# Performance work log

Hardware: AMD Instinct MI355X
Metric: run time of the kernel (lower is better)

Reference implementation:

```python
import jax, jax.numpy as jnp
import numpy as np

N_CELLS, IN_DIM, HID, OUT = 65536, 128, 256, 128
MLP_H = 128   # engine MLP hidden width is hard-coded to 128 in the source
N_MORPH = 32  # min(32, n_cells//4)


def setup_inputs() -> dict:
    key = jax.random.key(0)
    ks = jax.random.split(key, 18)
    s = 0.05
    return {
        "x": jax.random.normal(ks[0], (1, IN_DIM), jnp.float32),
        "hiddens": jax.random.normal(ks[1], (N_CELLS, HID), jnp.float32) * 0.1,
        "Wa1": jax.random.normal(ks[2], (MLP_H, IN_DIM + HID), jnp.float32) * s,
        "ba1": jax.random.normal(ks[3], (MLP_H,), jnp.float32) * s,
        "Wa2": jax.random.normal(ks[4], (OUT, MLP_H), jnp.float32) * s,
        "ba2": jax.random.normal(ks[5], (OUT,), jnp.float32) * s,
        "Wg1": jax.random.normal(ks[6], (MLP_H, IN_DIM + HID), jnp.float32) * s,
        "bg1": jax.random.normal(ks[7], (MLP_H,), jnp.float32) * s,
        "Wg2": jax.random.normal(ks[8], (OUT, MLP_H), jnp.float32) * s,
        "bg2": jax.random.normal(ks[9], (OUT,), jnp.float32) * s,
        "W_ih": jax.random.normal(ks[10], (3 * HID, OUT + 1), jnp.float32) * s,
        "W_hh": jax.random.normal(ks[11], (3 * HID, HID), jnp.float32) * s,
        "b_ih": jax.random.normal(ks[12], (3 * HID,), jnp.float32) * s,
        "b_hh": jax.random.normal(ks[13], (3 * HID,), jnp.float32) * s,
        "nat_w": jnp.eye(HID, dtype=jnp.float32),  # nn.init.eye_
        "morph_w": jax.random.normal(ks[14], (N_MORPH, HID, HID), jnp.float32) * 0.02,
        "morph_src": jax.random.randint(ks[15], (N_MORPH,), 0, N_CELLS, jnp.int32),
        "morph_tgt": jax.random.randint(ks[16], (N_MORPH,), 0, N_CELLS, jnp.int32),
        "step": 0,
    }


def _forward(x, hiddens, Wa1, ba1, Wa2, ba2, Wg1, bg1, Wg2, bg2,
             W_ih, W_hh, b_ih, b_hh, nat_w, morph_w, morph_src, morph_tgt, step):
    n = hiddens.shape[0]
    # --- BenchMind, batched over all cells (x broadcast to every cell) ---
    xb = jnp.broadcast_to(x, (n, x.shape[-1]))
    combined = jnp.concatenate([xb, hiddens], axis=-1)               # [n, in+hid]
    a = jax.nn.relu(combined @ Wa1.T + ba1) @ Wa2.T + ba2            # [n, out]
    g = jax.nn.relu(combined @ Wg1.T + bg1) @ Wg2.T + bg2            # [n, out]
    out = a - g                                                       # [n, out]
    tension = jnp.mean(out * out, axis=-1, keepdims=True)            # [n, 1]
    # mem_input is detached in torch
    mem_in = jax.lax.stop_gradient(jnp.concatenate([out, tension], axis=-1))
    # --- PyTorch GRUCell math ---
    gi = mem_in @ W_ih.T + b_ih                                      # [n, 3H]
    gh = hiddens @ W_hh.T + b_hh                                     # [n, 3H]
    i_r, i_z, i_n = jnp.split(gi, 3, axis=-1)
    h_r, h_z, h_n = jnp.split(gh, 3, axis=-1)
    r = jax.nn.sigmoid(i_r + h_r)
    z = jax.nn.sigmoid(i_z + h_z)
    nn_ = jnp.tanh(i_n + r * h_n)
    hid = jax.lax.stop_gradient((1.0 - z) * nn_ + z * hiddens)       # detached new hiddens
    if step % 3 == 0:
        hid = jax.lax.stop_gradient(hid @ nat_w.T)                   # natural transformation
    # --- limit / colimit (morphism gather-transform-aggregate) ---
    limit = jnp.einsum('mij,mj->i', morph_w, hid[morph_src]) / N_MORPH
    colimit = jnp.einsum('mji,mj->i', morph_w, hid[morph_tgt]) / N_MORPH
    diff = limit - colimit
    cat_tension = jnp.mean(diff * diff)
    hid = hid + 0.05 * jax.lax.stop_gradient(diff)[None, :]
    # --- faction sync (+ debate if step > 5) ---
    n_f = min(8, n // 2)
    fs = n // n_f
    hf = hid[: n_f * fs].reshape(n_f, fs, hid.shape[-1])
    fmean = hf.mean(axis=1, keepdims=True)                           # [n_f,1,H]
    hf = 0.85 * hf + 0.15 * fmean
    if step > 5:
        global_op = hf.mean(axis=1).mean(axis=0)                     # mean of faction means
        dc = max(1, fs // 4)
        hf = hf.at[:, :dc].set(0.85 * hf[:, :dc] + 0.15 * global_op)
    hid = jnp.concatenate([hf.reshape(n_f * fs, -1), hid[n_f * fs:]], axis=0)
    # --- tension-weighted combination (weights detached: .item() in torch) ---
    t = jax.lax.stop_gradient(tension[:, 0])                         # [n]
    w = jax.nn.softmax(t, axis=0)
    combined_out = jnp.sum(w[:, None] * out, axis=0, keepdims=True)  # [1, out]
    avg_tension = jnp.mean(tension) + 0.1 * cat_tension
    return combined_out, avg_tension, hid


def reference(x, hiddens, Wa1, ba1, Wa2, ba2, Wg1, bg1, Wg2, bg2,
              W_ih, W_hh, b_ih, b_hh, nat_w, morph_w, morph_src, morph_tgt, step):
    combined_out, avg_tension, _ = _forward(
        x, hiddens, Wa1, ba1, Wa2, ba2, Wg1, bg1, Wg2, bg2,
        W_ih, W_hh, b_ih, b_hh, nat_w, morph_w, morph_src, morph_tgt, step)
    return combined_out, avg_tension
```

## Files before the change

### kernel.cpp

```cpp
#include <hip/hip_runtime.h>
#include <math.h>

#define OFF_W1B   0
#define OFF_W2A   32768
#define OFF_XW1B  49152
#define OFF_B2D   49408
#define OFF_PT    49536
#define OFF_PE    51584
#define OFF_POUT  53632
#define OFF_MI4   315776
#define OFF_TEN   323968
#define OFF_HH4   324032
#define OFF_GI    340416
#define OFF_GH    389568
#define OFF_PLIM  438720
#define OFF_PCOL8 446912
#define OFF_GMSK  512448

typedef short bf16x8 __attribute__((ext_vector_type(8)));
typedef short s16x4  __attribute__((ext_vector_type(4)));
typedef float f32x4  __attribute__((ext_vector_type(4)));

__device__ __forceinline__ unsigned short f2bf(float f) {
    unsigned u = __builtin_bit_cast(unsigned, f);
    u += 0x7FFFu + ((u >> 16) & 1u);
    return (unsigned short)(u >> 16);
}

__device__ __forceinline__ bf16x8 cvt8(float4 a, float4 b) {
    bf16x8 v;
    v[0] = (short)f2bf(a.x); v[1] = (short)f2bf(a.y);
    v[2] = (short)f2bf(a.z); v[3] = (short)f2bf(a.w);
    v[4] = (short)f2bf(b.x); v[5] = (short)f2bf(b.y);
    v[6] = (short)f2bf(b.z); v[7] = (short)f2bf(b.w);
    return v;
}

__global__ __launch_bounds__(256) void k_prep(
    const float* __restrict__ x, const float* __restrict__ hiddens,
    const float* __restrict__ Wa1, const float* __restrict__ ba1,
    const float* __restrict__ Wa2, const float* __restrict__ ba2,
    const float* __restrict__ Wg1, const float* __restrict__ bg1,
    const float* __restrict__ Wg2, const float* __restrict__ bg2,
    const int* __restrict__ msrc, const int* __restrict__ mtgt,
    float* __restrict__ ws)
{
    const int b = blockIdx.x, t = threadIdx.x;
    unsigned short* w1b = (unsigned short*)(ws + OFF_W1B);
    unsigned short* w2a = (unsigned short*)(ws + OFF_W2A);
    if (b < 256) {
        const int n = b;
        const float* row = (n < 128) ? &Wa1[n * 384] : &Wg1[(n - 128) * 384];
        const int kc = t >> 3;
        w1b[(kc * 256 + n) * 8 + (t & 7)] = f2bf(row[128 + t]);
        if (n < 128) {
            float w2 = (t < 128) ? Wa2[n * 128 + t] : -Wg2[n * 128 + (t - 128)];
            w2a[(kc * 128 + n) * 8 + (t & 7)] = f2bf(w2);
        }
    } else if (b == 256) {
        const int n = t;
        const float* wr = (n < 128) ? &Wa1[n * 384] : &Wg1[(n - 128) * 384];
        float s = (n < 128) ? ba1[n] : bg1[n - 128];
        for (int j = 0; j < 128; ++j) s = fmaf(x[j], wr[j], s);
        ws[OFF_XW1B + n] = s;
        if (n < 128) ws[OFF_B2D + n] = ba2[n] - bg2[n];
    } else if (b == 257) {
        unsigned* gm = (unsigned*)(ws + OFF_GMSK);
        for (int i = t; i < 2048; i += 256) gm[i] = 0u;
        __syncthreads();
        if (t < 64) {
            const int cell = (t < 32) ? msrc[t] : mtgt[t - 32];
            atomicOr(&gm[cell >> 5], 1u << (cell & 31));
        }
    } else {
        const int g = b - 258;
        const int cell = (g < 32) ? msrc[g] : mtgt[g - 32];
        ws[OFF_HH4 + (t >> 2) * 256 + g * 4 + (t & 3)] = hiddens[(size_t)cell * 256 + t];
    }
}

__global__ __launch_bounds__(256, 2) void k_main(
    const float* __restrict__ hiddens,
    const int* __restrict__ msrc, const int* __restrict__ mtgt,
    float* __restrict__ ws)
{
    __shared__ __align__(16) short hB[32 * 256];
    __shared__ __align__(16) short h1B[32 * 256];
    __shared__ float part[128];
    __shared__ float e_sm[32], t_sm_[32];
    __shared__ int gid_sm[64];

    const int tid  = threadIdx.x;
    const int lane = tid & 63, wid = tid >> 6;
    const int l15 = lane & 15, l4 = lane >> 4;
    const int bt = blockIdx.x;

    if (tid < 64) gid_sm[tid] = (tid < 32) ? msrc[tid] : mtgt[tid - 32];

    const uint4* w1g = (const uint4*)(ws + OFF_W1B);
    const uint4* w2g = (const uint4*)(ws + OFF_W2A);
    const unsigned* gm = (const unsigned*)(ws + OFF_GMSK);

    {
        const int rc = tid >> 3;
        const float* hsrc = hiddens + (size_t)(bt * 32 + rc) * 256 + (tid & 7) * 32;
        float4 v0 = *(const float4*)(hsrc + 0);
        float4 v1 = *(const float4*)(hsrc + 4);
        float4 v2 = *(const float4*)(hsrc + 8);
        float4 v3 = *(const float4*)(hsrc + 12);
        float4 v4 = *(const float4*)(hsrc + 16);
        float4 v5 = *(const float4*)(hsrc + 20);
        float4 v6 = *(const float4*)(hsrc + 24);
        float4 v7 = *(const float4*)(hsrc + 28);
        const int kc0 = (tid & 7) * 4;
        *(bf16x8*)&hB[rc * 256 + (((kc0 + 0) ^ (rc & 15)) << 3)] = cvt8(v0, v1);
        *(bf16x8*)&hB[rc * 256 + (((kc0 + 1) ^ (rc & 15)) << 3)] = cvt8(v2, v3);
        *(bf16x8*)&hB[rc * 256 + (((kc0 + 2) ^ (rc & 15)) << 3)] = cvt8(v4, v5);
        *(bf16x8*)&hB[rc * 256 + (((kc0 + 3) ^ (rc & 15)) << 3)] = cvt8(v6, v7);
    }
    __syncthreads();

    const int wb1 = wid * 64 + l15;
    uint4 c0 = w1g[(0 + l4) * 256 + wb1 + 0];
    uint4 c1 = w1g[(0 + l4) * 256 + wb1 + 16];
    uint4 c2 = w1g[(0 + l4) * 256 + wb1 + 32];
    uint4 c3 = w1g[(0 + l4) * 256 + wb1 + 48];
    uint4 p0 = w1g[(4 + l4) * 256 + wb1 + 0];
    uint4 p1 = w1g[(4 + l4) * 256 + wb1 + 16];
    uint4 p2 = w1g[(4 + l4) * 256 + wb1 + 32];
    uint4 p3 = w1g[(4 + l4) * 256 + wb1 + 48];
    uint4 g2c0, g2c1, g2p0, g2p1;

    f32x4 acc[4][2];
#pragma unroll
    for (int q = 0; q < 4; ++q)
#pragma unroll
        for (int ct = 0; ct < 2; ++ct) acc[q][ct] = (f32x4)0.f;

    __builtin_amdgcn_s_setprio(1);
#pragma unroll
    for (int s = 0; s < 8; ++s) {
        uint4 f0, f1, f2, f3;
        if (s < 6) {
            f0 = w1g[((s + 2) * 4 + l4) * 256 + wb1 + 0];
            f1 = w1g[((s + 2) * 4 + l4) * 256 + wb1 + 16];
            f2 = w1g[((s + 2) * 4 + l4) * 256 + wb1 + 32];
            f3 = w1g[((s + 2) * 4 + l4) * 256 + wb1 + 48];
        } else if (s == 6) {
            g2c0 = w2g[(0 + l4) * 128 + wid * 32 + l15];
            g2c1 = w2g[(0 + l4) * 128 + wid * 32 + 16 + l15];
        } else {
            g2p0 = w2g[(4 + l4) * 128 + wid * 32 + l15];
            g2p1 = w2g[(4 + l4) * 128 + wid * 32 + 16 + l15];
        }
        bf16x8 bfr0 = *(const bf16x8*)&hB[(0 * 16 + l15) * 256 + (((s * 4 + l4) ^ l15) << 3)];
        bf16x8 bfr1 = *(const bf16x8*)&hB[(1 * 16 + l15) * 256 + (((s * 4 + l4) ^ l15) << 3)];
        acc[0][0] = __builtin_amdgcn_mfma_f32_16x16x32_bf16(__builtin_bit_cast(bf16x8, c0), bfr0, acc[0][0], 0, 0, 0);
        acc[0][1] = __builtin_amdgcn_mfma_f32_16x16x32_bf16(__builtin_bit_cast(bf16x8, c0), bfr1, acc[0][1], 0, 0, 0);
        acc[1][0] = __builtin_amdgcn_mfma_f32_16x16x32_bf16(__builtin_bit_cast(bf16x8, c1), bfr0, acc[1][0], 0, 0, 0);
        acc[1][1] = __builtin_amdgcn_mfma_f32_16x16x32_bf16(__builtin_bit_cast(bf16x8, c1), bfr1, acc[1][1], 0, 0, 0);
        acc[2][0] = __builtin_amdgcn_mfma_f32_16x16x32_bf16(__builtin_bit_cast(bf16x8, c2), bfr0, acc[2][0], 0, 0, 0);
        acc[2][1] = __builtin_amdgcn_mfma_f32_16x16x32_bf16(__builtin_bit_cast(bf16x8, c2), bfr1, acc[2][1], 0, 0, 0);
        acc[3][0] = __builtin_amdgcn_mfma_f32_16x16x32_bf16(__builtin_bit_cast(bf16x8, c3), bfr0, acc[3][0], 0, 0, 0);
        acc[3][1] = __builtin_amdgcn_mfma_f32_16x16x32_bf16(__builtin_bit_cast(bf16x8, c3), bfr1, acc[3][1], 0, 0, 0);
        c0 = p0; c1 = p1; c2 = p2; c3 = p3;
        if (s < 6) { p0 = f0; p1 = f1; p2 = f2; p3 = f3; }
    }
    __builtin_amdgcn_s_setprio(0);

#pragma unroll
    for (int nt = 0; nt < 4; ++nt) {
        const int n0 = wid * 64 + nt * 16 + l4 * 4;
        float4 xb = *(const float4*)(ws + OFF_XW1B + n0);
        const float bx[4] = {xb.x, xb.y, xb.z, xb.w};
        const int chunk = n0 >> 3;
        const int off = (l4 & 1) * 4;
#pragma unroll
        for (int ct = 0; ct < 2; ++ct) {
            const int c = ct * 16 + l15;
            s16x4 pk;
#pragma unroll
            for (int r = 0; r < 4; ++r)
                pk[r] = (short)f2bf(fmaxf(acc[nt][ct][r] + bx[r], 0.f));
            *(s16x4*)&h1B[c * 256 + ((chunk ^ l15) << 3) + off] = pk;
        }
    }
    __syncthreads();

    f32x4 acc2[2][2];
#pragma unroll
    for (int ot = 0; ot < 2; ++ot)
#pragma unroll
        for (int ct = 0; ct < 2; ++ct) acc2[ot][ct] = (f32x4)0.f;

    __builtin_amdgcn_s_setprio(1);
#pragma unroll
    for (int s = 0; s < 8; ++s) {
        uint4 f0, f1;
        if (s < 6) {
            f0 = w2g[((s + 2) * 4 + l4) * 128 + wid * 32 + l15];
            f1 = w2g[((s + 2) * 4 + l4) * 128 + wid * 32 + 16 + l15];
        }
        bf16x8 b20 = *(const bf16x8*)&h1B[(0 * 16 + l15) * 256 + (((s * 4 + l4) ^ l15) << 3)];
        bf16x8 b21 = *(const bf16x8*)&h1B[(1 * 16 + l15) * 256 + (((s * 4 + l4) ^ l15) << 3)];
        acc2[0][0] = __builtin_amdgcn_mfma_f32_16x16x32_bf16(__builtin_bit_cast(bf16x8, g2c0), b20, acc2[0][0], 0, 0, 0);
        acc2[0][1] = __builtin_amdgcn_mfma_f32_16x16x32_bf16(__builtin_bit_cast(bf16x8, g2c0), b21, acc2[0][1], 0, 0, 0);
        acc2[1][0] = __builtin_amdgcn_mfma_f32_16x16x32_bf16(__builtin_bit_cast(bf16x8, g2c1), b20, acc2[1][0], 0, 0, 0);
        acc2[1][1] = __builtin_amdgcn_mfma_f32_16x16x32_bf16(__builtin_bit_cast(bf16x8, g2c1), b21, acc2[1][1], 0, 0, 0);
        g2c0 = g2p0; g2c1 = g2p1;
        if (s < 6) { g2p0 = f0; g2p1 = f1; }
    }
    __builtin_amdgcn_s_setprio(0);

    float outv[2][2][4];
#pragma unroll
    for (int ot = 0; ot < 2; ++ot) {
        float4 bd = *(const float4*)(ws + OFF_B2D + wid * 32 + ot * 16 + l4 * 4);
        const float bv[4] = {bd.x, bd.y, bd.z, bd.w};
#pragma unroll
        for (int ct = 0; ct < 2; ++ct)
#pragma unroll
            for (int r = 0; r < 4; ++r)
                outv[ot][ct][r] = acc2[ot][ct][r] + bv[r];
    }

#pragma unroll
    for (int ct = 0; ct < 2; ++ct) {
        float sq = 0.f;
#pragma unroll
        for (int ot = 0; ot < 2; ++ot)
#pragma unroll
            for (int r = 0; r < 4; ++r)
                sq = fmaf(outv[ot][ct][r], outv[ot][ct][r], sq);
        sq += __shfl_xor(sq, 16);
        sq += __shfl_xor(sq, 32);
        if (l4 == 0) part[wid * 32 + ct * 16 + l15] = sq;
    }
    __syncthreads();

    if (tid < 32) {
        float s = part[tid] + part[32 + tid] + part[64 + tid] + part[96 + tid];
        const float tv = s * (1.f / 128.f);
        const float ev = expf(tv);
        t_sm_[tid] = tv; e_sm[tid] = ev;
        float pt = tv, pe = ev;
        for (int off = 16; off > 0; off >>= 1) {
            pt += __shfl_down(pt, off);
            pe += __shfl_down(pe, off);
        }
        if (tid == 0) { ws[OFF_PT + bt] = pt; ws[OFF_PE + bt] = pe; }
        unsigned m = gm[bt];
        while (m) {
            const int g = __builtin_ctz(m); m &= m - 1;
            const int cg = gid_sm[g];
            if ((cg >> 5) == bt && (cg & 31) == tid) ws[OFF_TEN + g] = tv;
        }
    }
    __syncthreads();

    {
        float p[2][4];
#pragma unroll
        for (int ot = 0; ot < 2; ++ot)
#pragma unroll
            for (int r = 0; r < 4; ++r) {
                float s = e_sm[l15] * outv[ot][0][r];
                s = fmaf(e_sm[16 + l15], outv[ot][1][r], s);
                p[ot][r] = s;
            }
#pragma unroll
        for (int ot = 0; ot < 2; ++ot)
#pragma unroll
            for (int r = 0; r < 4; ++r) {
                p[ot][r] += __shfl_xor(p[ot][r], 1);
                p[ot][r] += __shfl_xor(p[ot][r], 2);
                p[ot][r] += __shfl_xor(p[ot][r], 4);
                p[ot][r] += __shfl_xor(p[ot][r], 8);
            }
        if (l15 == 0) {
#pragma unroll
            for (int ot = 0; ot < 2; ++ot)
                *(float4*)(ws + OFF_POUT + (size_t)bt * 128 + wid * 32 + ot * 16 + l4 * 4) =
                    make_float4(p[ot][0], p[ot][1], p[ot][2], p[ot][3]);
        }
    }
    {
        unsigned m = gm[bt];
        while (m) {
            const int g = __builtin_ctz(m); m &= m - 1;
            const int cg = gid_sm[g];
            if ((cg >> 5) != bt) continue;
            const int c = cg & 31;
            if ((c & 15) == l15) {
                const int ct = c >> 4;
#pragma unroll
                for (int ot = 0; ot < 2; ++ot)
                    *(float4*)(ws + OFF_MI4 + (wid * 8 + ot * 4 + l4) * 256 + g * 4) =
                        make_float4(outv[ot][ct][0], outv[ot][ct][1],
                                    outv[ot][ct][2], outv[ot][ct][3]);
            }
        }
    }
}

__global__ __launch_bounds__(256) void k_tail1(
    const float* __restrict__ W_ih, const float* __restrict__ W_hh,
    const float* __restrict__ b_ih, const float* __restrict__ b_hh,
    float* __restrict__ ws)
{
    const int lane = threadIdx.x & 63;
    const int w    = threadIdx.x >> 6;
    const int row  = __builtin_amdgcn_readfirstlane(blockIdx.x * 4 + w);
    const float* mi4 = ws + OFF_MI4;
    const float* hh4 = ws + OFF_HH4;

    const float* wi = W_ih + row * 129;
    float gi = b_ih[row];
#pragma unroll 8
    for (int q = 0; q < 32; ++q) {
        float4 a = *(const float4*)(mi4 + q * 256 + lane * 4);
        gi = fmaf(wi[4 * q + 0], a.x, gi);
        gi = fmaf(wi[4 * q + 1], a.y, gi);
        gi = fmaf(wi[4 * q + 2], a.z, gi);
        gi = fmaf(wi[4 * q + 3], a.w, gi);
    }
    gi = fmaf(ws[OFF_TEN + lane], wi[128], gi);

    const float* wh = W_hh + (size_t)row * 256;
    float gh = b_hh[row];
#pragma unroll 8
    for (int q = 0; q < 64; ++q) {
        float4 a = *(const float4*)(hh4 + q * 256 + lane * 4);
        float4 b = *(const float4*)(wh + 4 * q);
        gh = fmaf(b.x, a.x, gh);
        gh = fmaf(b.y, a.y, gh);
        gh = fmaf(b.z, a.z, gh);
        gh = fmaf(b.w, a.w, gh);
    }
    ws[OFF_GI + lane * 768 + row] = gi;
    ws[OFF_GH + lane * 768 + row] = gh;
}

__global__ __launch_bounds__(256) void k_morph(
    const float* __restrict__ morph_w, const float* __restrict__ nat_w,
    const int* __restrict__ step, float* __restrict__ ws)
{
    __shared__ float wsm[32 * 264];
    __shared__ float hd0[256], hd1[256];
    __shared__ float hs[256], ht[256];
    const int blk = blockIdx.x, t = threadIdx.x;
    const int m = blk >> 3, ch = blk & 7;
    const float* wm = morph_w + (size_t)m * 65536 + (size_t)ch * 32 * 256;
    {
        const int r = t >> 3, c0 = (t & 7) * 32;
#pragma unroll
        for (int it = 0; it < 8; ++it)
            *(float4*)&wsm[r * 264 + c0 + it * 4] = *(const float4*)(wm + r * 256 + c0 + it * 4);
    }
#pragma unroll
    for (int h = 0; h < 2; ++h) {
        const int g = h * 32 + m;
        const float i_r = ws[OFF_GI + g * 768 + t];
        const float i_z = ws[OFF_GI + g * 768 + 256 + t];
        const float i_n = ws[OFF_GI + g * 768 + 512 + t];
        const float h_r = ws[OFF_GH + g * 768 + t];
        const float h_z = ws[OFF_GH + g * 768 + 256 + t];
        const float h_n = ws[OFF_GH + g * 768 + 512 + t];
        const float hv  = ws[OFF_HH4 + (t >> 2) * 256 + g * 4 + (t & 3)];
        const float r  = 1.f / (1.f + expf(-(i_r + h_r)));
        const float z  = 1.f / (1.f + expf(-(i_z + h_z)));
        const float nn = tanhf(i_n + r * h_n);
        const float hid = (1.f - z) * nn + z * hv;
        if (h == 0) hd0[t] = hid; else hd1[t] = hid;
    }
    __syncthreads();

    float hn0, hn1;
    if (step[0] % 3 == 0) {
        const float4* wr = (const float4*)(nat_w + (size_t)t * 256);
        float s0 = 0.f, s1 = 0.f;
        for (int q = 0; q < 64; ++q) {
            float4 wq = wr[q];
            s0 = fmaf(wq.x, hd0[4 * q + 0], s0); s1 = fmaf(wq.x, hd1[4 * q + 0], s1);
            s0 = fmaf(wq.y, hd0[4 * q + 1], s0); s1 = fmaf(wq.y, hd1[4 * q + 1], s1);
            s0 = fmaf(wq.z, hd0[4 * q + 2], s0); s1 = fmaf(wq.z, hd1[4 * q + 2], s1);
            s0 = fmaf(wq.w, hd0[4 * q + 3], s0); s1 = fmaf(wq.w, hd1[4 * q + 3], s1);
        }
        hn0 = s0; hn1 = s1;
    } else {
        hn0 = hd0[t]; hn1 = hd1[t];
    }
    hs[t] = hn0; ht[t] = hn1;
    __syncthreads();

    {
        const int il = t >> 3, jc = t & 7;
        float L = 0.f;
#pragma unroll 8
        for (int jj = 0; jj < 32; ++jj) {
            const int j = jc + 8 * jj;
            L = fmaf(wsm[il * 264 + j], hs[j], L);
        }
        L += __shfl_down(L, 4);
        L += __shfl_down(L, 2);
        L += __shfl_down(L, 1);
        if (jc == 0) ws[OFF_PLIM + m * 256 + ch * 32 + il] = L;
    }
    {
        float C = 0.f;
#pragma unroll 8
        for (int r = 0; r < 32; ++r)
            C = fmaf(wsm[r * 264 + t], ht[ch * 32 + r], C);
        ws[OFF_PCOL8 + blk * 256 + t] = C;
    }
}

__global__ __launch_bounds__(256) void k_out(const float* __restrict__ ws,
                                             float* __restrict__ out)
{
    __shared__ float red[256];
    const int b = blockIdx.x, t = threadIdx.x;
    if (b < 128) {
        float so = 0.f, se = 0.f;
        for (int i = t; i < 2048; i += 256) {
            so += ws[OFF_POUT + (size_t)i * 128 + b];
            se += ws[OFF_PE + i];
        }
        red[t] = so; __syncthreads();
        for (int s = 128; s > 0; s >>= 1) { if (t < s) red[t] += red[t + s]; __syncthreads(); }
        const float SO = red[0]; __syncthreads();
        red[t] = se; __syncthreads();
        for (int s = 128; s > 0; s >>= 1) { if (t < s) red[t] += red[t + s]; __syncthreads(); }
        if (t == 0) out[b] = SO / red[0];
    } else {
        float pt = 0.f;
        for (int i = t; i < 2048; i += 256) pt += ws[OFF_PT + i];
        float L = 0.f, C = 0.f;
        for (int m = 0; m < 32; ++m) L += ws[OFF_PLIM + m * 256 + t];
        for (int mc = 0; mc < 256; ++mc) C += ws[OFF_PCOL8 + mc * 256 + t];
        const float d = (L - C) * (1.f / 32.f);
        red[t] = d * d; __syncthreads();
        for (int s = 128; s > 0; s >>= 1) { if (t < s) red[t] += red[t + s]; __syncthreads(); }
        const float cat = red[0] * (1.f / 256.f); __syncthreads();
        red[t] = pt; __syncthreads();
        for (int s = 128; s > 0; s >>= 1) { if (t < s) red[t] += red[t + s]; __syncthreads(); }
        if (t == 0) out[128] = red[0] * (1.f / 65536.f) + 0.1f * cat;
    }
}

extern "C" void kernel_launch(void* const* d_in, const int* in_sizes, int n_in,
                              void* d_out, int out_size, void* d_ws, size_t ws_size,
                              hipStream_t stream)
{
    const float* x     = (const float*)d_in[0];
    const float* hidd  = (const float*)d_in[1];
    const float* Wa1   = (const float*)d_in[2];
    const float* ba1   = (const float*)d_in[3];
    const float* Wa2   = (const float*)d_in[4];
    const float* ba2   = (const float*)d_in[5];
    const float* Wg1   = (const float*)d_in[6];
    const float* bg1   = (const float*)d_in[7];
    const float* Wg2   = (const float*)d_in[8];
    const float* bg2   = (const float*)d_in[9];
    const float* W_ih  = (const float*)d_in[10];
    const float* W_hh  = (const float*)d_in[11];
    const float* b_ih  = (const float*)d_in[12];
    const float* b_hh  = (const float*)d_in[13];
    const float* nat_w = (const float*)d_in[14];
    const float* mw    = (const float*)d_in[15];
    const int*   msrc  = (const int*)d_in[16];
    const int*   mtgt  = (const int*)d_in[17];
    const int*   step  = (const int*)d_in[18];

    float* out = (float*)d_out;
    float* ws  = (float*)d_ws;

    k_prep <<<322, 256, 0, stream>>>(x, hidd, Wa1, ba1, Wa2, ba2, Wg1, bg1, Wg2, bg2, msrc, mtgt, ws);
    k_main <<<2048, 256, 0, stream>>>(hidd, msrc, mtgt, ws);
    k_tail1<<<192, 256, 0, stream>>>(W_ih, W_hh, b_ih, b_hh, ws);
    k_morph<<<256, 256, 0, stream>>>(mw, nat_w, step, ws);
    k_out  <<<129, 256, 0, stream>>>(ws, out);
}
```

Before: 76.17 us.

## Process two 32-cell tiles per k_main block with prefetched second tile

Each k_main block now handles 64 cells as two sequential 32-row tiles, halving the grid to 1024 blocks. The second tile's hidden rows are loaded into registers at the start and converted into a second LDS buffer while the first tile's layer-1 epilogue runs, so their load latency overlaps compute. Launch bounds are raised to 3 blocks per SM. The cost is more LDS per block, higher register pressure from the prefetched values, and fewer blocks for latency hiding.

Measured after the change: 82.87 us. +8.8%, slower.

```diff
diff --git a/kernel.cpp b/kernel.cpp
--- a/kernel.cpp
+++ b/kernel.cpp
@@ -79,12 +79,12 @@
     }
 }
 
-__global__ __launch_bounds__(256, 2) void k_main(
+__global__ __launch_bounds__(256, 3) void k_main(
     const float* __restrict__ hiddens,
     const int* __restrict__ msrc, const int* __restrict__ mtgt,
     float* __restrict__ ws)
 {
-    __shared__ __align__(16) short hB[32 * 256];
+    __shared__ __align__(16) short hB[2][32 * 256];
     __shared__ __align__(16) short h1B[32 * 256];
     __shared__ float part[128];
     __shared__ float e_sm[32], t_sm_[32];
@@ -93,7 +93,7 @@
     const int tid  = threadIdx.x;
     const int lane = tid & 63, wid = tid >> 6;
     const int l15 = lane & 15, l4 = lane >> 4;
-    const int bt = blockIdx.x;
+    const int blk = blockIdx.x;
 
     if (tid < 64) gid_sm[tid] = (tid < 32) ? msrc[tid] : mtgt[tid - 32];
 
@@ -101,9 +101,11 @@
     const uint4* w2g = (const uint4*)(ws + OFF_W2A);
     const unsigned* gm = (const unsigned*)(ws + OFF_GMSK);
 
+    const int rc = tid >> 3;
+    const int kc0 = (tid & 7) * 4;
+    const float* hsrc = hiddens + (size_t)(blk * 64 + rc) * 256 + (tid & 7) * 32;
+
     {
-        const int rc = tid >> 3;
-        const float* hsrc = hiddens + (size_t)(bt * 32 + rc) * 256 + (tid & 7) * 32;
         float4 v0 = *(const float4*)(hsrc + 0);
         float4 v1 = *(const float4*)(hsrc + 4);
         float4 v2 = *(const float4*)(hsrc + 8);
@@ -112,194 +114,215 @@
         float4 v5 = *(const float4*)(hsrc + 20);
         float4 v6 = *(const float4*)(hsrc + 24);
         float4 v7 = *(const float4*)(hsrc + 28);
-        const int kc0 = (tid & 7) * 4;
-        *(bf16x8*)&hB[rc * 256 + (((kc0 + 0) ^ (rc & 15)) << 3)] = cvt8(v0, v1);
-        *(bf16x8*)&hB[rc * 256 + (((kc0 + 1) ^ (rc & 15)) << 3)] = cvt8(v2, v3);
-        *(bf16x8*)&hB[rc * 256 + (((kc0 + 2) ^ (rc & 15)) << 3)] = cvt8(v4, v5);
-        *(bf16x8*)&hB[rc * 256 + (((kc0 + 3) ^ (rc & 15)) << 3)] = cvt8(v6, v7);
-    }
+        *(bf16x8*)&hB[0][rc * 256 + (((kc0 + 0) ^ (rc & 15)) << 3)] = cvt8(v0, v1);
+        *(bf16x8*)&hB[0][rc * 256 + (((kc0 + 1) ^ (rc & 15)) << 3)] = cvt8(v2, v3);
+        *(bf16x8*)&hB[0][rc * 256 + (((kc0 + 2) ^ (rc & 15)) << 3)] = cvt8(v4, v5);
+        *(bf16x8*)&hB[0][rc * 256 + (((kc0 + 3) ^ (rc & 15)) << 3)] = cvt8(v6, v7);
+    }
+    float4 n0 = *(const float4*)(hsrc + 8192 + 0);
+    float4 n1 = *(const float4*)(hsrc + 8192 + 4);
+    float4 n2 = *(const float4*)(hsrc + 8192 + 8);
+    float4 n3 = *(const float4*)(hsrc + 8192 + 12);
+    float4 n4 = *(const float4*)(hsrc + 8192 + 16);
+    float4 n5 = *(const float4*)(hsrc + 8192 + 20);
+    float4 n6 = *(const float4*)(hsrc + 8192 + 24);
+    float4 n7 = *(const float4*)(hsrc + 8192 + 28);
     __syncthreads();
 
     const int wb1 = wid * 64 + l15;
-    uint4 c0 = w1g[(0 + l4) * 256 + wb1 + 0];
-    uint4 c1 = w1g[(0 + l4) * 256 + wb1 + 16];
-    uint4 c2 = w1g[(0 + l4) * 256 + wb1 + 32];
-    uint4 c3 = w1g[(0 + l4) * 256 + wb1 + 48];
-    uint4 p0 = w1g[(4 + l4) * 256 + wb1 + 0];
-    uint4 p1 = w1g[(4 + l4) * 256 + wb1 + 16];
-    uint4 p2 = w1g[(4 + l4) * 256 + wb1 + 32];
-    uint4 p3 = w1g[(4 + l4) * 256 + wb1 + 48];
-    uint4 g2c0, g2c1, g2p0, g2p1;
-
-    f32x4 acc[4][2];
-#pragma unroll
-    for (int q = 0; q < 4; ++q)
-#pragma unroll
-        for (int ct = 0; ct < 2; ++ct) acc[q][ct] = (f32x4)0.f;
-
-    __builtin_amdgcn_s_setprio(1);
-#pragma unroll
-    for (int s = 0; s < 8; ++s) {
-        uint4 f0, f1, f2, f3;
-        if (s < 6) {
-            f0 = w1g[((s + 2) * 4 + l4) * 256 + wb1 + 0];
-            f1 = w1g[((s + 2) * 4 + l4) * 256 + wb1 + 16];
-            f2 = w1g[((s + 2) * 4 + l4) * 256 + wb1 + 32];
-            f3 = w1g[((s + 2) * 4 + l4) * 256 + wb1 + 48];
-        } else if (s == 6) {
-            g2c0 = w2g[(0 + l4) * 128 + wid * 32 + l15];
-            g2c1 = w2g[(0 + l4) * 128 + wid * 32 + 16 + l15];
-        } else {
-            g2p0 = w2g[(4 + l4) * 128 + wid * 32 + l15];
-            g2p1 = w2g[(4 + l4) * 128 + wid * 32 + 16 + l15];
-        }
-        bf16x8 bfr0 = *(const bf16x8*)&hB[(0 * 16 + l15) * 256 + (((s * 4 + l4) ^ l15) << 3)];
-        bf16x8 bfr1 = *(const bf16x8*)&hB[(1 * 16 + l15) * 256 + (((s * 4 + l4) ^ l15) << 3)];
-        acc[0][0] = __builtin_amdgcn_mfma_f32_16x16x32_bf16(__builtin_bit_cast(bf16x8, c0), bfr0, acc[0][0], 0, 0, 0);
-        acc[0][1] = __builtin_amdgcn_mfma_f32_16x16x32_bf16(__builtin_bit_cast(bf16x8, c0), bfr1, acc[0][1], 0, 0, 0);
-        acc[1][0] = __builtin_amdgcn_mfma_f32_16x16x32_bf16(__builtin_bit_cast(bf16x8, c1), bfr0, acc[1][0], 0, 0, 0);
-        acc[1][1] = __builtin_amdgcn_mfma_f32_16x16x32_bf16(__builtin_bit_cast(bf16x8, c1), bfr1, acc[1][1], 0, 0, 0);
-        acc[2][0] = __builtin_amdgcn_mfma_f32_16x16x32_bf16(__builtin_bit_cast(bf16x8, c2), bfr0, acc[2][0], 0, 0, 0);
-        acc[2][1] = __builtin_amdgcn_mfma_f32_16x16x32_bf16(__builtin_bit_cast(bf16x8, c2), bfr1, acc[2][1], 0, 0, 0);
-        acc[3][0] = __builtin_amdgcn_mfma_f32_16x16x32_bf16(__builtin_bit_cast(bf16x8, c3), bfr0, acc[3][0], 0, 0, 0);
-        acc[3][1] = __builtin_amdgcn_mfma_f32_16x16x32_bf16(__builtin_bit_cast(bf16x8, c3), bfr1, acc[3][1], 0, 0, 0);
-        c0 = p0; c1 = p1; c2 = p2; c3 = p3;
-        if (s < 6) { p0 = f0; p1 = f1; p2 = f2; p3 = f3; }
-    }
-    __builtin_amdgcn_s_setprio(0);
-
-#pragma unroll
-    for (int nt = 0; nt < 4; ++nt) {
-        const int n0 = wid * 64 + nt * 16 + l4 * 4;
-        float4 xb = *(const float4*)(ws + OFF_XW1B + n0);
-        const float bx[4] = {xb.x, xb.y, xb.z, xb.w};
-        const int chunk = n0 >> 3;
-        const int off = (l4 & 1) * 4;
+
+#pragma unroll
+    for (int t = 0; t < 2; ++t) {
+        const int bt = blk * 2 + t;
+        const short* hBt = hB[t];
+
+        uint4 c0 = w1g[(0 + l4) * 256 + wb1 + 0];
+        uint4 c1 = w1g[(0 + l4) * 256 + wb1 + 16];
+        uint4 c2 = w1g[(0 + l4) * 256 + wb1 + 32];
+        uint4 c3 = w1g[(0 + l4) * 256 + wb1 + 48];
+        uint4 p0 = w1g[(4 + l4) * 256 + wb1 + 0];
+        uint4 p1 = w1g[(4 + l4) * 256 + wb1 + 16];
+        uint4 p2 = w1g[(4 + l4) * 256 + wb1 + 32];
+        uint4 p3 = w1g[(4 + l4) * 256 + wb1 + 48];
+        uint4 g2c0, g2c1, g2p0, g2p1;
+
+        f32x4 acc[4][2];
+#pragma unroll
+        for (int q = 0; q < 4; ++q)
+#pragma unroll
+            for (int ct = 0; ct < 2; ++ct) acc[q][ct] = (f32x4)0.f;
+
+        __builtin_amdgcn_s_setprio(1);
+#pragma unroll
+        for (int s = 0; s < 8; ++s) {
+            uint4 f0, f1, f2, f3;
+            if (s < 6) {
+                f0 = w1g[((s + 2) * 4 + l4) * 256 + wb1 + 0];
+                f1 = w1g[((s + 2) * 4 + l4) * 256 + wb1 + 16];
+                f2 = w1g[((s + 2) * 4 + l4) * 256 + wb1 + 32];
+                f3 = w1g[((s + 2) * 4 + l4) * 256 + wb1 + 48];
+            } else if (s == 6) {
+                g2c0 = w2g[(0 + l4) * 128 + wid * 32 + l15];
+                g2c1 = w2g[(0 + l4) * 128 + wid * 32 + 16 + l15];
+            } else {
+                g2p0 = w2g[(4 + l4) * 128 + wid * 32 + l15];
+                g2p1 = w2g[(4 + l4) * 128 + wid * 32 + 16 + l15];
+            }
+            bf16x8 bfr0 = *(const bf16x8*)&hBt[(0 * 16 + l15) * 256 + (((s * 4 + l4) ^ l15) << 3)];
+            bf16x8 bfr1 = *(const bf16x8*)&hBt[(1 * 16 + l15) * 256 + (((s * 4 + l4) ^ l15) << 3)];
+            acc[0][0] = __builtin_amdgcn_mfma_f32_16x16x32_bf16(__builtin_bit_cast(bf16x8, c0), bfr0, acc[0][0], 0, 0, 0);
+            acc[0][1] = __builtin_amdgcn_mfma_f32_16x16x32_bf16(__builtin_bit_cast(bf16x8, c0), bfr1, acc[0][1], 0, 0, 0);
+            acc[1][0] = __builtin_amdgcn_mfma_f32_16x16x32_bf16(__builtin_bit_cast(bf16x8, c1), bfr0, acc[1][0], 0, 0, 0);
+            acc[1][1] = __builtin_amdgcn_mfma_f32_16x16x32_bf16(__builtin_bit_cast(bf16x8, c1), bfr1, acc[1][1], 0, 0, 0);
+            acc[2][0] = __builtin_amdgcn_mfma_f32_16x16x32_bf16(__builtin_bit_cast(bf16x8, c2), bfr0, acc[2][0], 0, 0, 0);
+            acc[2][1] = __builtin_amdgcn_mfma_f32_16x16x32_bf16(__builtin_bit_cast(bf16x8, c2), bfr1, acc[2][1], 0, 0, 0);
+            acc[3][0] = __builtin_amdgcn_mfma_f32_16x16x32_bf16(__builtin_bit_cast(bf16x8, c3), bfr0, acc[3][0], 0, 0, 0);
+            acc[3][1] = __builtin_amdgcn_mfma_f32_16x16x32_bf16(__builtin_bit_cast(bf16x8, c3), bfr1, acc[3][1], 0, 0, 0);
+            c0 = p0; c1 = p1; c2 = p2; c3 = p3;
+            if (s < 6) { p0 = f0; p1 = f1; p2 = f2; p3 = f3; }
+        }
+        __builtin_amdgcn_s_setprio(0);
+
+#pragma unroll
+        for (int nt = 0; nt < 4; ++nt) {
+            const int n0i = wid * 64 + nt * 16 + l4 * 4;
+            float4 xb = *(const float4*)(ws + OFF_XW1B + n0i);
+            const float bx[4] = {xb.x, xb.y, xb.z, xb.w};
+            const int chunk = n0i >> 3;
+            const int off = (l4 & 1) * 4;
+#pragma unroll
+            for (int ct = 0; ct < 2; ++ct) {
+                const int c = ct * 16 + l15;
+                s16x4 pk;
+#pragma unroll
+                for (int r = 0; r < 4; ++r)
+                    pk[r] = (short)f2bf(fmaxf(acc[nt][ct][r] + bx[r], 0.f));
+                *(s16x4*)&h1B[c * 256 + ((chunk ^ l15) << 3) + off] = pk;
+            }
+        }
+        if (t == 0) {
+            *(bf16x8*)&hB[1][rc * 256 + (((kc0 + 0) ^ (rc & 15)) << 3)] = cvt8(n0, n1);
+            *(bf16x8*)&hB[1][rc * 256 + (((kc0 + 1) ^ (rc & 15)) << 3)] = cvt8(n2, n3);
+            *(bf16x8*)&hB[1][rc * 256 + (((kc0 + 2) ^ (rc & 15)) << 3)] = cvt8(n4, n5);
+            *(bf16x8*)&hB[1][rc * 256 + (((kc0 + 3) ^ (rc & 15)) << 3)] = cvt8(n6, n7);
+        }
+        __syncthreads();
+
+        f32x4 acc2[2][2];
+#pragma unroll
+        for (int ot = 0; ot < 2; ++ot)
+#pragma unroll
+            for (int ct = 0; ct < 2; ++ct) acc2[ot][ct] = (f32x4)0.f;
+
+        __builtin_amdgcn_s_setprio(1);
+#pragma unroll
+        for (int s = 0; s < 8; ++s) {
+            uint4 f0, f1;
+            if (s < 6) {
+                f0 = w2g[((s + 2) * 4 + l4) * 128 + wid * 32 + l15];
+                f1 = w2g[((s + 2) * 4 + l4) * 128 + wid * 32 + 16 + l15];
+            }
+            bf16x8 b20 = *(const bf16x8*)&h1B[(0 * 16 + l15) * 256 + (((s * 4 + l4) ^ l15) << 3)];
+            bf16x8 b21 = *(const bf16x8*)&h1B[(1 * 16 + l15) * 256 + (((s * 4 + l4) ^ l15) << 3)];
+            acc2[0][0] = __builtin_amdgcn_mfma_f32_16x16x32_bf16(__builtin_bit_cast(bf16x8, g2c0), b20, acc2[0][0], 0, 0, 0);
+            acc2[0][1] = __builtin_amdgcn_mfma_f32_16x16x32_bf16(__builtin_bit_cast(bf16x8, g2c0), b21, acc2[0][1], 0, 0, 0);
+            acc2[1][0] = __builtin_amdgcn_mfma_f32_16x16x32_bf16(__builtin_bit_cast(bf16x8, g2c1), b20, acc2[1][0], 0, 0, 0);
+            acc2[1][1] = __builtin_amdgcn_mfma_f32_16x16x32_bf16(__builtin_bit_cast(bf16x8, g2c1), b21, acc2[1][1], 0, 0, 0);
+            g2c0 = g2p0; g2c1 = g2p1;
+            if (s < 6) { g2p0 = f0; g2p1 = f1; }
+        }
+        __builtin_amdgcn_s_setprio(0);
+
+        float outv[2][2][4];
+#pragma unroll
+        for (int ot = 0; ot < 2; ++ot) {
+            float4 bd = *(const float4*)(ws + OFF_B2D + wid * 32 + ot * 16 + l4 * 4);
+            const float bv[4] = {bd.x, bd.y, bd.z, bd.w};
+#pragma unroll
+            for (int ct = 0; ct < 2; ++ct)
+#pragma unroll
+                for (int r = 0; r < 4; ++r)
+                    outv[ot][ct][r] = acc2[ot][ct][r] + bv[r];
+        }
+
 #pragma unroll
         for (int ct = 0; ct < 2; ++ct) {
-            const int c = ct * 16 + l15;
-            s16x4 pk;
-#pragma unroll
-            for (int r = 0; r < 4; ++r)
-                pk[r] = (short)f2bf(fmaxf(acc[nt][ct][r] + bx[r], 0.f));
-            *(s16x4*)&h1B[c * 256 + ((chunk ^ l15) << 3) + off] = pk;
-        }
-    }
-    __syncthreads();
-
-    f32x4 acc2[2][2];
-#pragma unroll
-    for (int ot = 0; ot < 2; ++ot)
-#pragma unroll
-        for (int ct = 0; ct < 2; ++ct) acc2[ot][ct] = (f32x4)0.f;
-
-    __builtin_amdgcn_s_setprio(1);
-#pragma unroll
-    for (int s = 0; s < 8; ++s) {
-        uint4 f0, f1;
-        if (s < 6) {
-            f0 = w2g[((s + 2) * 4 + l4) * 128 + wid * 32 + l15];
-            f1 = w2g[((s + 2) * 4 + l4) * 128 + wid * 32 + 16 + l15];
-        }
-        bf16x8 b20 = *(const bf16x8*)&h1B[(0 * 16 + l15) * 256 + (((s * 4 + l4) ^ l15) << 3)];
-        bf16x8 b21 = *(const bf16x8*)&h1B[(1 * 16 + l15) * 256 + (((s * 4 + l4) ^ l15) << 3)];
-        acc2[0][0] = __builtin_amdgcn_mfma_f32_16x16x32_bf16(__builtin_bit_cast(bf16x8, g2c0), b20, acc2[0][0], 0, 0, 0);
-        acc2[0][1] = __builtin_amdgcn_mfma_f32_16x16x32_bf16(__builtin_bit_cast(bf16x8, g2c0), b21, acc2[0][1], 0, 0, 0);
-        acc2[1][0] = __builtin_amdgcn_mfma_f32_16x16x32_bf16(__builtin_bit_cast(bf16x8, g2c1), b20, acc2[1][0], 0, 0, 0);
-        acc2[1][1] = __builtin_amdgcn_mfma_f32_16x16x32_bf16(__builtin_bit_cast(bf16x8, g2c1), b21, acc2[1][1], 0, 0, 0);
-        g2c0 = g2p0; g2c1 = g2p1;
-        if (s < 6) { g2p0 = f0; g2p1 = f1; }
-    }
-    __builtin_amdgcn_s_setprio(0);
-
-    float outv[2][2][4];
-#pragma unroll
-    for (int ot = 0; ot < 2; ++ot) {
-        float4 bd = *(const float4*)(ws + OFF_B2D + wid * 32 + ot * 16 + l4 * 4);
-        const float bv[4] = {bd.x, bd.y, bd.z, bd.w};
-#pragma unroll
-        for (int ct = 0; ct < 2; ++ct)
-#pragma unroll
-            for (int r = 0; r < 4; ++r)
-                outv[ot][ct][r] = acc2[ot][ct][r] + bv[r];
-    }
-
-#pragma unroll
-    for (int ct = 0; ct < 2; ++ct) {
-        float sq = 0.f;
-#pragma unroll
-        for (int ot = 0; ot < 2; ++ot)
-#pragma unroll
-            for (int r = 0; r < 4; ++r)
-                sq = fmaf(outv[ot][ct][r], outv[ot][ct][r], sq);
-        sq += __shfl_xor(sq, 16);
-        sq += __shfl_xor(sq, 32);
-        if (l4 == 0) part[wid * 32 + ct * 16 + l15] = sq;
-    }
-    __syncthreads();
-
-    if (tid < 32) {
-        float s = part[tid] + part[32 + tid] + part[64 + tid] + part[96 + tid];
-        const float tv = s * (1.f / 128.f);
-        const float ev = expf(tv);
-        t_sm_[tid] = tv; e_sm[tid] = ev;
-        float pt = tv, pe = ev;
-        for (int off = 16; off > 0; off >>= 1) {
-            pt += __shfl_down(pt, off);
-            pe += __shfl_down(pe, off);
-        }
-        if (tid == 0) { ws[OFF_PT + bt] = pt; ws[OFF_PE + bt] = pe; }
-        unsigned m = gm[bt];
-        while (m) {
-            const int g = __builtin_ctz(m); m &= m - 1;
-            const int cg = gid_sm[g];
-            if ((cg >> 5) == bt && (cg & 31) == tid) ws[OFF_TEN + g] = tv;
-        }
-    }
-    __syncthreads();
-
-    {
-        float p[2][4];
-#pragma unroll
-        for (int ot = 0; ot < 2; ++ot)
-#pragma unroll
-            for (int r = 0; r < 4; ++r) {
-                float s = e_sm[l15] * outv[ot][0][r];
-                s = fmaf(e_sm[16 + l15], outv[ot][1][r], s);
-                p[ot][r] = s;
-            }
-#pragma unroll
-        for (int ot = 0; ot < 2; ++ot)
-#pragma unroll
-            for (int r = 0; r < 4; ++r) {
-                p[ot][r] += __shfl_xor(p[ot][r], 1);
-                p[ot][r] += __shfl_xor(p[ot][r], 2);
-                p[ot][r] += __shfl_xor(p[ot][r], 4);
-                p[ot][r] += __shfl_xor(p[ot][r], 8);
-            }
-        if (l15 == 0) {
+            float sq = 0.f;
 #pragma unroll
             for (int ot = 0; ot < 2; ++ot)
-                *(float4*)(ws + OFF_POUT + (size_t)bt * 128 + wid * 32 + ot * 16 + l4 * 4) =
-                    make_float4(p[ot][0], p[ot][1], p[ot][2], p[ot][3]);
-        }
-    }
-    {
-        unsigned m = gm[bt];
-        while (m) {
-            const int g = __builtin_ctz(m); m &= m - 1;
-            const int cg = gid_sm[g];
-            if ((cg >> 5) != bt) continue;
-            const int c = cg & 31;
-            if ((c & 15) == l15) {
-                const int ct = c >> 4;
+#pragma unroll
+                for (int r = 0; r < 4; ++r)
+                    sq = fmaf(outv[ot][ct][r], outv[ot][ct][r], sq);
+            sq += __shfl_xor(sq, 16);
+            sq += __shfl_xor(sq, 32);
+            if (l4 == 0) part[wid * 32 + ct * 16 + l15] = sq;
+        }
+        __syncthreads();
+
+        if (tid < 32) {
+            float s = part[tid] + part[32 + tid] + part[64 + tid] + part[96 + tid];
+            const float tv = s * (1.f / 128.f);
+            const float ev = expf(tv);
+            t_sm_[tid] = tv; e_sm[tid] = ev;
+            float pt = tv, pe = ev;
+            for (int off = 16; off > 0; off >>= 1) {
+                pt += __shfl_down(pt, off);
+                pe += __shfl_down(pe, off);
+            }
+            if (tid == 0) { ws[OFF_PT + bt] = pt; ws[OFF_PE + bt] = pe; }
+            unsigned m = gm[bt];
+            while (m) {
+                const int g = __builtin_ctz(m); m &= m - 1;
+                const int cg = gid_sm[g];
+                if ((cg >> 5) == bt && (cg & 31) == tid) ws[OFF_TEN + g] = tv;
+            }
+        }
+        __syncthreads();
+
+        {
+            float p[2][4];
+#pragma unroll
+            for (int ot = 0; ot < 2; ++ot)
+#pragma unroll
+                for (int r = 0; r < 4; ++r) {
+                    float s = e_sm[l15] * outv[ot][0][r];
+                    s = fmaf(e_sm[16 + l15], outv[ot][1][r], s);
+                    p[ot][r] = s;
+                }
+#pragma unroll
+            for (int ot = 0; ot < 2; ++ot)
+#pragma unroll
+                for (int r = 0; r < 4; ++r) {
+                    p[ot][r] += __shfl_xor(p[ot][r], 1);
+                    p[ot][r] += __shfl_xor(p[ot][r], 2);
+                    p[ot][r] += __shfl_xor(p[ot][r], 4);
+                    p[ot][r] += __shfl_xor(p[ot][r], 8);
+                }
+            if (l15 == 0) {
 #pragma unroll
                 for (int ot = 0; ot < 2; ++ot)
-                    *(float4*)(ws + OFF_MI4 + (wid * 8 + ot * 4 + l4) * 256 + g * 4) =
-                        make_float4(outv[ot][ct][0], outv[ot][ct][1],
-                                    outv[ot][ct][2], outv[ot][ct][3]);
-            }
-        }
+                    *(float4*)(ws + OFF_POUT + (size_t)bt * 128 + wid * 32 + ot * 16 + l4 * 4) =
+                        make_float4(p[ot][0], p[ot][1], p[ot][2], p[ot][3]);
+            }
+        }
+        {
+            unsigned m = gm[bt];
+            while (m) {
+                const int g = __builtin_ctz(m); m &= m - 1;
+                const int cg = gid_sm[g];
+                if ((cg >> 5) != bt) continue;
+                const int c = cg & 31;
+                if ((c & 15) == l15) {
+                    const int ct = c >> 4;
+#pragma unroll
+                    for (int ot = 0; ot < 2; ++ot)
+                        *(float4*)(ws + OFF_MI4 + (wid * 8 + ot * 4 + l4) * 256 + g * 4) =
+                            make_float4(outv[ot][ct][0], outv[ot][ct][1],
+                                        outv[ot][ct][2], outv[ot][ct][3]);
+                }
+            }
+        }
+        if (t == 0) __syncthreads();
     }
 }
 
@@ -476,7 +499,7 @@
     float* ws  = (float*)d_ws;
 
     k_prep <<<322, 256, 0, stream>>>(x, hidd, Wa1, ba1, Wa2, ba2, Wg1, bg1, Wg2, bg2, msrc, mtgt, ws);
-    k_main <<<2048, 256, 0, stream>>>(hidd, msrc, mtgt, ws);
+    k_main <<<1024, 256, 0, stream>>>(hidd, msrc, mtgt, ws);
     k_tail1<<<192, 256, 0, stream>>>(W_ih, W_hh, b_ih, b_hh, ws);
     k_morph<<<256, 256, 0, stream>>>(mw, nat_w, step, ws);
     k_out  <<<129, 256, 0, stream>>>(ws, out);
```

## Stream hiddens directly from global into MFMA operands, drop LDS staging

Applied to the files above, without the earlier changes.

Removes the shared-memory staging buffer for the hidden-state tile: each lane now loads its fp32 hidden slices straight from global memory one k-step ahead and converts them to bf16 in registers right before the MFMA. The weight prefetch depth drops from two stages to one, and the second-layer weights are fetched in the last iteration's prefetch slot. Freeing the LDS buffer and the extra prefetch registers is meant to allow three blocks per CU instead of two and removes a block-wide barrier. The trade-off is less latency hiding per wave, and global hidden loads that are less coalesced (lanes stride across 16 rows).

After: 97.91 us. 1.29x slower.

```diff
diff --git a/kernel.cpp b/kernel.cpp
--- a/kernel.cpp
+++ b/kernel.cpp
@@ -79,12 +79,11 @@
     }
 }
 
-__global__ __launch_bounds__(256, 2) void k_main(
+__global__ __launch_bounds__(256, 3) void k_main(
     const float* __restrict__ hiddens,
     const int* __restrict__ msrc, const int* __restrict__ mtgt,
     float* __restrict__ ws)
 {
-    __shared__ __align__(16) short hB[32 * 256];
     __shared__ __align__(16) short h1B[32 * 256];
     __shared__ float part[128];
     __shared__ float e_sm[32], t_sm_[32];
@@ -101,34 +100,17 @@
     const uint4* w2g = (const uint4*)(ws + OFF_W2A);
     const unsigned* gm = (const unsigned*)(ws + OFF_GMSK);
 
-    {
-        const int rc = tid >> 3;
-        const float* hsrc = hiddens + (size_t)(bt * 32 + rc) * 256 + (tid & 7) * 32;
-        float4 v0 = *(const float4*)(hsrc + 0);
-        float4 v1 = *(const float4*)(hsrc + 4);
-        float4 v2 = *(const float4*)(hsrc + 8);
-        float4 v3 = *(const float4*)(hsrc + 12);
-        float4 v4 = *(const float4*)(hsrc + 16);
-        float4 v5 = *(const float4*)(hsrc + 20);
-        float4 v6 = *(const float4*)(hsrc + 24);
-        float4 v7 = *(const float4*)(hsrc + 28);
-        const int kc0 = (tid & 7) * 4;
-        *(bf16x8*)&hB[rc * 256 + (((kc0 + 0) ^ (rc & 15)) << 3)] = cvt8(v0, v1);
-        *(bf16x8*)&hB[rc * 256 + (((kc0 + 1) ^ (rc & 15)) << 3)] = cvt8(v2, v3);
-        *(bf16x8*)&hB[rc * 256 + (((kc0 + 2) ^ (rc & 15)) << 3)] = cvt8(v4, v5);
-        *(bf16x8*)&hB[rc * 256 + (((kc0 + 3) ^ (rc & 15)) << 3)] = cvt8(v6, v7);
-    }
-    __syncthreads();
+    const float* hc0 = hiddens + (size_t)(bt * 32 + l15) * 256 + l4 * 8;
+    const float* hc1 = hc0 + 16 * 256;
 
     const int wb1 = wid * 64 + l15;
     uint4 c0 = w1g[(0 + l4) * 256 + wb1 + 0];
     uint4 c1 = w1g[(0 + l4) * 256 + wb1 + 16];
     uint4 c2 = w1g[(0 + l4) * 256 + wb1 + 32];
     uint4 c3 = w1g[(0 + l4) * 256 + wb1 + 48];
-    uint4 p0 = w1g[(4 + l4) * 256 + wb1 + 0];
-    uint4 p1 = w1g[(4 + l4) * 256 + wb1 + 16];
-    uint4 p2 = w1g[(4 + l4) * 256 + wb1 + 32];
-    uint4 p3 = w1g[(4 + l4) * 256 + wb1 + 48];
+    float4 b0a0 = *(const float4*)(hc0 + 0), b0b0 = *(const float4*)(hc0 + 4);
+    float4 b1a0 = *(const float4*)(hc1 + 0), b1b0 = *(const float4*)(hc1 + 4);
+
     uint4 g2c0, g2c1, g2p0, g2p1;
 
     f32x4 acc[4][2];
@@ -141,20 +123,26 @@
 #pragma unroll
     for (int s = 0; s < 8; ++s) {
         uint4 f0, f1, f2, f3;
-        if (s < 6) {
-            f0 = w1g[((s + 2) * 4 + l4) * 256 + wb1 + 0];
-            f1 = w1g[((s + 2) * 4 + l4) * 256 + wb1 + 16];
-            f2 = w1g[((s + 2) * 4 + l4) * 256 + wb1 + 32];
-            f3 = w1g[((s + 2) * 4 + l4) * 256 + wb1 + 48];
-        } else if (s == 6) {
-            g2c0 = w2g[(0 + l4) * 128 + wid * 32 + l15];
-            g2c1 = w2g[(0 + l4) * 128 + wid * 32 + 16 + l15];
+        if (s < 7) {
+            f0 = w1g[((s + 1) * 4 + l4) * 256 + wb1 + 0];
+            f1 = w1g[((s + 1) * 4 + l4) * 256 + wb1 + 16];
+            f2 = w1g[((s + 1) * 4 + l4) * 256 + wb1 + 32];
+            f3 = w1g[((s + 1) * 4 + l4) * 256 + wb1 + 48];
         } else {
-            g2p0 = w2g[(4 + l4) * 128 + wid * 32 + l15];
-            g2p1 = w2g[(4 + l4) * 128 + wid * 32 + 16 + l15];
-        }
-        bf16x8 bfr0 = *(const bf16x8*)&hB[(0 * 16 + l15) * 256 + (((s * 4 + l4) ^ l15) << 3)];
-        bf16x8 bfr1 = *(const bf16x8*)&hB[(1 * 16 + l15) * 256 + (((s * 4 + l4) ^ l15) << 3)];
+            f0 = w2g[(0 + l4) * 128 + wid * 32 + l15];
+            f1 = w2g[(0 + l4) * 128 + wid * 32 + 16 + l15];
+            f2 = w2g[(4 + l4) * 128 + wid * 32 + l15];
+            f3 = w2g[(4 + l4) * 128 + wid * 32 + 16 + l15];
+        }
+        float4 nb0a, nb0b, nb1a, nb1b;
+        if (s < 7) {
+            nb0a = *(const float4*)(hc0 + (s + 1) * 32);
+            nb0b = *(const float4*)(hc0 + (s + 1) * 32 + 4);
+            nb1a = *(const float4*)(hc1 + (s + 1) * 32);
+            nb1b = *(const float4*)(hc1 + (s + 1) * 32 + 4);
+        }
+        const bf16x8 bfr0 = cvt8(b0a0, b0b0);
+        const bf16x8 bfr1 = cvt8(b1a0, b1b0);
         acc[0][0] = __builtin_amdgcn_mfma_f32_16x16x32_bf16(__builtin_bit_cast(bf16x8, c0), bfr0, acc[0][0], 0, 0, 0);
         acc[0][1] = __builtin_amdgcn_mfma_f32_16x16x32_bf16(__builtin_bit_cast(bf16x8, c0), bfr1, acc[0][1], 0, 0, 0);
         acc[1][0] = __builtin_amdgcn_mfma_f32_16x16x32_bf16(__builtin_bit_cast(bf16x8, c1), bfr0, acc[1][0], 0, 0, 0);
@@ -163,10 +151,11 @@
         acc[2][1] = __builtin_amdgcn_mfma_f32_16x16x32_bf16(__builtin_bit_cast(bf16x8, c2), bfr1, acc[2][1], 0, 0, 0);
         acc[3][0] = __builtin_amdgcn_mfma_f32_16x16x32_bf16(__builtin_bit_cast(bf16x8, c3), bfr0, acc[3][0], 0, 0, 0);
         acc[3][1] = __builtin_amdgcn_mfma_f32_16x16x32_bf16(__builtin_bit_cast(bf16x8, c3), bfr1, acc[3][1], 0, 0, 0);
-        c0 = p0; c1 = p1; c2 = p2; c3 = p3;
-        if (s < 6) { p0 = f0; p1 = f1; p2 = f2; p3 = f3; }
+        c0 = f0; c1 = f1; c2 = f2; c3 = f3;
+        if (s < 7) { b0a0 = nb0a; b0b0 = nb0b; b1a0 = nb1a; b1b0 = nb1b; }
     }
     __builtin_amdgcn_s_setprio(0);
+    g2c0 = c0; g2c1 = c1; g2p0 = c2; g2p1 = c3;
 
 #pragma unroll
     for (int nt = 0; nt < 4; ++nt) {
```
